# Kernel tuning notes

Measured on AMD Instinct MI355X. Metric: run time of the kernel, lower is better.

## Reference

```python
import jax, jax.numpy as jnp
import numpy as np

NUM_HEADS = 16
TEMPERATURE = 0.2


def setup_inputs() -> dict:
    key = jax.random.key(0)
    ks = jax.random.split(key, 6)
    B, TGT, SRC, D = 8, 256, 512, 1024
    seqs = jax.random.normal(ks[0], (B, TGT, D), jnp.float32)
    keys = jax.random.normal(ks[1], (B, SRC, D), jnp.float32)
    scale = 1.0 / np.sqrt(D).astype(np.float32)
    q_w = jax.random.normal(ks[2], (D, D), jnp.float32) * scale
    q_b = jax.random.normal(ks[3], (D,), jnp.float32) * 0.01
    k_w = jax.random.normal(ks[4], (D, D), jnp.float32) * scale
    k_b = jax.random.normal(ks[5], (D,), jnp.float32) * 0.01
    energy_bias = jnp.full((1,), -0.5, jnp.float32)
    return {"seqs": seqs, "keys": keys, "q_w": q_w, "q_b": q_b,
            "k_w": k_w, "k_b": k_b, "energy_bias": energy_bias}


def _monotonic_alignment(p):
    # p: (BH, tgt, src). Faithful to torch: T_i = triu(cumprod(1 - triu(roll(p_i),1)))
    # but T is built per target step inside a scan instead of materializing
    # the full (BH, tgt, src, src) tensor.
    BH, T, S = p.shape
    idx = jnp.arange(S)
    mask_strict = idx[None, :] > idx[:, None]   # triu(1)
    mask_ge = idx[None, :] >= idx[:, None]      # triu(0)
    p_roll = jnp.roll(p, 1, axis=-1)

    def step_T(pr_i):  # pr_i: (BH, S) -> (BH, S, S)
        pe = jnp.where(mask_strict, pr_i[:, None, :], 0.0)
        return jnp.where(mask_ge, jnp.cumprod(1.0 - pe, axis=-1), 0.0)

    T0 = step_T(p_roll[:, 0])
    alpha0 = p[:, 0] * T0[:, 0, :]              # (BH, S)

    def scan_fn(alpha, xs):
        p_i, pr_i = xs
        Ti = step_T(pr_i)                        # (BH, S, S)
        alpha_new = p_i * jnp.einsum('bm,bmn->bn', alpha, Ti)
        return alpha_new, alpha_new

    _, alphas = jax.lax.scan(
        scan_fn, alpha0,
        (jnp.swapaxes(p[:, 1:], 0, 1), jnp.swapaxes(p_roll[:, 1:], 0, 1)))
    return jnp.concatenate([alpha0[:, None], jnp.swapaxes(alphas, 0, 1)], axis=1)


def reference(seqs, keys, q_w, q_b, k_w, k_b, energy_bias):
    B, TGT, D = seqs.shape
    SRC = keys.shape[1]
    H = NUM_HEADS
    dh = D // H
    # EnergyProjection with num_layers=1: Linear + ReLU
    q = jax.nn.relu(seqs @ q_w.T + q_b)
    k = jax.nn.relu(keys @ k_w.T + k_b)
    q = q.reshape(B, TGT, H, dh).transpose(0, 2, 1, 3)   # (B,H,tgt,dh)
    k = k.reshape(B, SRC, H, dh).transpose(0, 2, 1, 3)   # (B,H,src,dh)
    energy = jnp.einsum('bhtd,bhsd->bhts', q, k) * (dh ** -0.5) + energy_bias[0]
    p_choose = jax.nn.sigmoid(energy / TEMPERATURE)       # (B,H,tgt,src)
    alpha = _monotonic_alignment(p_choose.reshape(B * H, TGT, SRC))
    alpha = alpha.reshape(B, H, TGT, SRC)
    return p_choose, alpha
```

## Files before the change

kernel.cpp:

```cpp
#include <hip/hip_runtime.h>

#define B_   8
#define TGT_ 256
#define SRC_ 512
#define D_   1024
#define H_   16
#define DH_  64

typedef _Float16 half4 __attribute__((ext_vector_type(4)));
typedef _Float16 half8 __attribute__((ext_vector_type(8)));
typedef float    floatx4 __attribute__((ext_vector_type(4)));

template <int CTRL>
__device__ __forceinline__ float dppf(float x) {
    return __int_as_float(__builtin_amdgcn_update_dpp(
        0, __float_as_int(x), CTRL, 0xF, 0xF, true));
}
__device__ __forceinline__ float rdlane(float x, int lane) {
    return __int_as_float(__builtin_amdgcn_readlane(__float_as_int(x), lane));
}

__global__ __launch_bounds__(256) void proj_fused_kernel(
    const float* __restrict__ seqs, const float* __restrict__ keys,
    const float* __restrict__ q_w,  const float* __restrict__ k_w,
    const float* __restrict__ q_b,  const float* __restrict__ k_b,
    _Float16* __restrict__ Qh, _Float16* __restrict__ Kh)
{
    __shared__ _Float16 As[128 * 32];
    __shared__ _Float16 Ws[64 * 32];

    const int tid = threadIdx.x;
    const int bx  = blockIdx.x;
    const int K   = D_;
    const int N   = D_;

    const float* A; const float* W; const float* bias; _Float16* C;
    int bm0;
    if (bx < 16) { A = seqs; W = q_w; bias = q_b; C = Qh; bm0 = bx * 128; }
    else         { A = keys; W = k_w; bias = k_b; C = Kh; bm0 = (bx - 16) * 128; }
    const int bn0 = blockIdx.y * 64;

    const int lrow = tid >> 3;
    const int lkc  = (tid & 7) * 4;
    const float* aG = A + (size_t)(bm0 + lrow) * K + lkc;
    const float* wG = W + (size_t)(bn0 + lrow) * K + lkc;
    _Float16* aL = As + tid * 4;
    _Float16* wL = Ws + tid * 4;

    float4 ra[4], rw[2];
#define PROJ_LOAD(k0)                                                       \
    {                                                                       \
        ra[0] = *(const float4*)(aG + (k0));                                \
        ra[1] = *(const float4*)(aG + (size_t)32 * K + (k0));               \
        ra[2] = *(const float4*)(aG + (size_t)64 * K + (k0));               \
        ra[3] = *(const float4*)(aG + (size_t)96 * K + (k0));               \
        rw[0] = *(const float4*)(wG + (k0));                                \
        rw[1] = *(const float4*)(wG + (size_t)32 * K + (k0));               \
    }

    floatx4 acc[4][2];
#pragma unroll
    for (int i = 0; i < 4; ++i)
#pragma unroll
        for (int j = 0; j < 2; ++j) acc[i][j] = (floatx4){0.f, 0.f, 0.f, 0.f};

    const int lane = tid & 63;
    const int wid  = tid >> 6;
    const int wm   = (wid >> 1) * 64;
    const int wn   = (wid & 1) * 32;
    const int fm   = lane & 15;
    const int fk   = (lane >> 4) * 8;
    const _Float16* aF = As + (wm + fm) * 32 + fk;
    const _Float16* bF = Ws + (wn + fm) * 32 + fk;

    PROJ_LOAD(0);

    for (int k0 = 0; k0 < K; k0 += 32) {
        __syncthreads();
#pragma unroll
        for (int i = 0; i < 4; ++i) {
            half4 h = { (_Float16)ra[i].x, (_Float16)ra[i].y,
                        (_Float16)ra[i].z, (_Float16)ra[i].w };
            *(half4*)(aL + i * 1024) = h;
        }
#pragma unroll
        for (int i = 0; i < 2; ++i) {
            half4 h = { (_Float16)rw[i].x, (_Float16)rw[i].y,
                        (_Float16)rw[i].z, (_Float16)rw[i].w };
            *(half4*)(wL + i * 1024) = h;
        }
        if (k0 + 32 < K) PROJ_LOAD(k0 + 32);
        __syncthreads();

        half8 a0 = *(const half8*)(aF);
        half8 a1 = *(const half8*)(aF + 16 * 32);
        half8 a2 = *(const half8*)(aF + 32 * 32);
        half8 a3 = *(const half8*)(aF + 48 * 32);
        half8 b0 = *(const half8*)(bF);
        half8 b1 = *(const half8*)(bF + 16 * 32);

        acc[0][0] = __builtin_amdgcn_mfma_f32_16x16x32_f16(a0, b0, acc[0][0], 0, 0, 0);
        acc[1][0] = __builtin_amdgcn_mfma_f32_16x16x32_f16(a1, b0, acc[1][0], 0, 0, 0);
        acc[2][0] = __builtin_amdgcn_mfma_f32_16x16x32_f16(a2, b0, acc[2][0], 0, 0, 0);
        acc[3][0] = __builtin_amdgcn_mfma_f32_16x16x32_f16(a3, b0, acc[3][0], 0, 0, 0);
        acc[0][1] = __builtin_amdgcn_mfma_f32_16x16x32_f16(a0, b1, acc[0][1], 0, 0, 0);
        acc[1][1] = __builtin_amdgcn_mfma_f32_16x16x32_f16(a1, b1, acc[1][1], 0, 0, 0);
        acc[2][1] = __builtin_amdgcn_mfma_f32_16x16x32_f16(a2, b1, acc[2][1], 0, 0, 0);
        acc[3][1] = __builtin_amdgcn_mfma_f32_16x16x32_f16(a3, b1, acc[3][1], 0, 0, 0);
    }

    const int er = (lane >> 4) * 4;
#pragma unroll
    for (int nt = 0; nt < 2; ++nt) {
        const int col = bn0 + wn + nt * 16 + fm;
        const float bv = bias[col];
#pragma unroll
        for (int mt = 0; mt < 4; ++mt) {
            const int row0 = bm0 + wm + mt * 16 + er;
#pragma unroll
            for (int r = 0; r < 4; ++r) {
                float v = acc[mt][nt][r] + bv;
                v = fmaxf(v, 0.0f);
                C[(size_t)(row0 + r) * N + col] = (_Float16)v;
            }
        }
    }
#undef PROJ_LOAD
}

__global__ __launch_bounds__(256) void energy_mfma_kernel(
    const _Float16* __restrict__ Q, const _Float16* __restrict__ K,
    const float* __restrict__ eb_ptr, float* __restrict__ P)
{
    __shared__ __align__(16) _Float16 Qt[2 * 64 * 32];
    __shared__ __align__(16) _Float16 Kt[2 * 128 * 32];

    const int tid = threadIdx.x;
    const int bh  = blockIdx.x;
    const int b   = bh >> 4;
    const int h   = bh & 15;
    const int t0  = blockIdx.y << 6;
    const int s0  = blockIdx.z << 7;

#pragma unroll
    for (int u = 0; u < 2; ++u) {
        const int unit = tid + u * 256;
        const int row = unit >> 3, hc = unit & 7;
        half8 v = *(const half8*)(Q + ((size_t)(b * TGT_ + t0 + row)) * D_ + h * DH_ + hc * 8);
        *(half8*)(Qt + (hc >> 2) * (64 * 32) + row * 32 + (hc & 3) * 8) = v;
    }
#pragma unroll
    for (int u = 0; u < 4; ++u) {
        const int unit = tid + u * 256;
        const int row = unit >> 3, hc = unit & 7;
        half8 v = *(const half8*)(K + ((size_t)(b * SRC_ + s0 + row)) * D_ + h * DH_ + hc * 8);
        *(half8*)(Kt + (hc >> 2) * (128 * 32) + row * 32 + (hc & 3) * 8) = v;
    }
    __syncthreads();

    const int lane = tid & 63;
    const int wid  = tid >> 6;
    const int wm   = (wid >> 1) * 32;
    const int wn   = (wid & 1) * 64;
    const int fm   = lane & 15;
    const int fk   = (lane >> 4) * 8;

    floatx4 acc[2][4];
#pragma unroll
    for (int i = 0; i < 2; ++i)
#pragma unroll
        for (int j = 0; j < 4; ++j) acc[i][j] = (floatx4){0.f, 0.f, 0.f, 0.f};

#pragma unroll
    for (int ks = 0; ks < 2; ++ks) {
        const _Float16* aB = Qt + ks * (64 * 32) + (wm + fm) * 32 + fk;
        const _Float16* bB = Kt + ks * (128 * 32) + (wn + fm) * 32 + fk;
        half8 a0 = *(const half8*)(aB);
        half8 a1 = *(const half8*)(aB + 16 * 32);
        half8 b0 = *(const half8*)(bB);
        half8 b1 = *(const half8*)(bB + 16 * 32);
        half8 b2 = *(const half8*)(bB + 32 * 32);
        half8 b3 = *(const half8*)(bB + 48 * 32);
        acc[0][0] = __builtin_amdgcn_mfma_f32_16x16x32_f16(a0, b0, acc[0][0], 0, 0, 0);
        acc[0][1] = __builtin_amdgcn_mfma_f32_16x16x32_f16(a0, b1, acc[0][1], 0, 0, 0);
        acc[0][2] = __builtin_amdgcn_mfma_f32_16x16x32_f16(a0, b2, acc[0][2], 0, 0, 0);
        acc[0][3] = __builtin_amdgcn_mfma_f32_16x16x32_f16(a0, b3, acc[0][3], 0, 0, 0);
        acc[1][0] = __builtin_amdgcn_mfma_f32_16x16x32_f16(a1, b0, acc[1][0], 0, 0, 0);
        acc[1][1] = __builtin_amdgcn_mfma_f32_16x16x32_f16(a1, b1, acc[1][1], 0, 0, 0);
        acc[1][2] = __builtin_amdgcn_mfma_f32_16x16x32_f16(a1, b2, acc[1][2], 0, 0, 0);
        acc[1][3] = __builtin_amdgcn_mfma_f32_16x16x32_f16(a1, b3, acc[1][3], 0, 0, 0);
    }

    const float eb = eb_ptr[0];
    const int er = (lane >> 4) * 4;
#pragma unroll
    for (int mt = 0; mt < 2; ++mt) {
#pragma unroll
        for (int nt = 0; nt < 4; ++nt) {
            const int s = s0 + wn + nt * 16 + fm;
#pragma unroll
            for (int r = 0; r < 4; ++r) {
                const int t = t0 + wm + mt * 16 + er + r;
                float x = (acc[mt][nt][r] * 0.125f + eb) * 5.0f;
                float p = 1.0f / (1.0f + __expf(-x));
                P[((size_t)bh * TGT_ + t) * SRC_ + s] = p;
            }
        }
    }
}

__global__ __launch_bounds__(64) void align_kernel(
    const float* __restrict__ P, float* __restrict__ Alpha)
{
    const int bh   = blockIdx.x;
    const int lane = threadIdx.x;
    const float* prow = P + (size_t)bh * TGT_ * SRC_;
    float* arow       = Alpha + (size_t)bh * TGT_ * SRC_;
    const int n0 = lane << 3;

    float bprev[8];
#pragma unroll
    for (int j = 0; j < 8; ++j) bprev[j] = 0.0f;
    if (lane == 0) bprev[0] = 1.0f;

    float4 bufA[8], bufB[8];
#pragma unroll
    for (int j = 0; j < 8; ++j) {
        const float* r = prow + (size_t)j * SRC_ + n0;
        bufA[j] = *(const float4*)r;
        bufB[j] = *(const float4*)(r + 4);
    }

    for (int g = 0; g < TGT_ / 8; ++g) {
#pragma unroll
        for (int jj = 0; jj < 8; ++jj) {
            const int i = g * 8 + jj;
            float4 ca = bufA[jj], cb = bufB[jj];
            if (g < TGT_ / 8 - 1) {
                const float* r = prow + (size_t)(i + 8) * SRC_ + n0;
                bufA[jj] = *(const float4*)r;
                bufB[jj] = *(const float4*)(r + 4);
            }
            float pl[8] = {ca.x, ca.y, ca.z, ca.w, cb.x, cb.y, cb.z, cb.w};

            float pm1 = dppf<0x111>(pl[7]);
            {
                float r15 = rdlane(pl[7], 15);
                float r31 = rdlane(pl[7], 31);
                float r47 = rdlane(pl[7], 47);
                pm1 = (lane == 16) ? r15 : pm1;
                pm1 = (lane == 32) ? r31 : pm1;
                pm1 = (lane == 48) ? r47 : pm1;
            }
            float a[8];
            a[0] = (lane == 0) ? 0.0f : (1.0f - pm1);
#pragma unroll
            for (int j = 1; j < 8; ++j) a[j] = 1.0f - pl[j - 1];

            float Aj[8], Bj[8];
            float A = a[0], Bv = bprev[0];
            Aj[0] = A; Bj[0] = Bv;
#pragma unroll
            for (int j = 1; j < 8; ++j) {
                Bv = fmaf(a[j], Bv, bprev[j]);
                A  = a[j] * A;
                Aj[j] = A; Bj[j] = Bv;
            }

            float As_ = A, Bs = Bv;
            {
                float Ash, Bsh;
                Ash = dppf<0x111>(As_); Bsh = dppf<0x111>(Bs);
                Ash = ((lane & 15) >= 1) ? Ash : 1.0f;
                Bs  = fmaf(As_, Bsh, Bs); As_ = As_ * Ash;
                Ash = dppf<0x112>(As_); Bsh = dppf<0x112>(Bs);
                Ash = ((lane & 15) >= 2) ? Ash : 1.0f;
                Bs  = fmaf(As_, Bsh, Bs); As_ = As_ * Ash;
                Ash = dppf<0x114>(As_); Bsh = dppf<0x114>(Bs);
                Ash = ((lane & 15) >= 4) ? Ash : 1.0f;
                Bs  = fmaf(As_, Bsh, Bs); As_ = As_ * Ash;
                Ash = dppf<0x118>(As_); Bsh = dppf<0x118>(Bs);
                Ash = ((lane & 15) >= 8) ? Ash : 1.0f;
                Bs  = fmaf(As_, Bsh, Bs); As_ = As_ * Ash;
            }

            float PB;
            {
                float B15 = rdlane(Bs, 15);
                float A31 = rdlane(As_, 31), B31 = rdlane(Bs, 31);
                float B47 = rdlane(Bs, 47);
                float PB1 = B15;
                float PB2 = fmaf(A31, PB1, B31);
                float PB3 = fmaf(rdlane(As_, 47), PB2, B47);
                const int seg = lane >> 4;
                PB = (seg == 0) ? 0.0f : ((seg == 1) ? PB1 : ((seg == 2) ? PB2 : PB3));
            }

            float EA = dppf<0x111>(As_);
            float EB = dppf<0x111>(Bs);
            EA = (lane & 15) ? EA : 1.0f;
            float cin = fmaf(EA, PB, EB);

            float an[8];
#pragma unroll
            for (int j = 0; j < 8; ++j) {
                float c = fmaf(Aj[j], cin, Bj[j]);
                an[j] = pl[j] * c;
                bprev[j] = an[j];
            }
            float4 o0 = {an[0], an[1], an[2], an[3]};
            float4 o1 = {an[4], an[5], an[6], an[7]};
            float* dst = arow + (size_t)i * SRC_ + n0;
            *(float4*)dst       = o0;
            *(float4*)(dst + 4) = o1;
        }
    }
}

extern "C" void kernel_launch(void* const* d_in, const int* in_sizes, int n_in,
                              void* d_out, int out_size, void* d_ws, size_t ws_size,
                              hipStream_t stream) {
    const float* seqs = (const float*)d_in[0];
    const float* keys = (const float*)d_in[1];
    const float* q_w  = (const float*)d_in[2];
    const float* q_b  = (const float*)d_in[3];
    const float* k_w  = (const float*)d_in[4];
    const float* k_b  = (const float*)d_in[5];
    const float* eb   = (const float*)d_in[6];

    float* out   = (float*)d_out;
    float* P     = out;
    float* Alpha = out + (size_t)B_ * H_ * TGT_ * SRC_;

    _Float16* Qh = (_Float16*)d_ws;
    _Float16* Kh = Qh + (size_t)B_ * TGT_ * D_;

    {
        dim3 grid(48, D_ / 64);
        proj_fused_kernel<<<grid, 256, 0, stream>>>(seqs, keys, q_w, k_w,
                                                    q_b, k_b, Qh, Kh);
    }
    {
        dim3 grid(B_ * H_, TGT_ / 64, SRC_ / 128);
        energy_mfma_kernel<<<grid, 256, 0, stream>>>(Qh, Kh, eb, P);
    }
    align_kernel<<<dim3(B_ * H_), 64, 0, stream>>>(P, Alpha);
}
```

Baseline: 234.4 us.

## Pre-convert inputs to fp16, use async LDS loads, stage energy stores through LDS

A separate conversion kernel turns the inputs and weights into fp16. The projection GEMM then loads fp16 tiles straight into LDS with global_load_lds and uses a larger 128x128 tile with 4x4 MFMA accumulators per wave. The energy kernel now writes sigmoid outputs through an LDS transpose buffer so the global stores become coalesced float4 rows. These changes add an extra kernel launch and an extra round trip through memory for the converted inputs, and the projection loop no longer has register prefetch overlap.

Result: no change. 233.3 us (-0.5%).

```diff
diff --git a/kernel.cpp b/kernel.cpp
--- a/kernel.cpp
+++ b/kernel.cpp
@@ -11,6 +11,12 @@
 typedef _Float16 half8 __attribute__((ext_vector_type(8)));
 typedef float    floatx4 __attribute__((ext_vector_type(4)));
 
+__device__ __forceinline__ void async_ld16(const void* g, void* l) {
+    __builtin_amdgcn_global_load_lds(
+        (const __attribute__((address_space(1))) void*)g,
+        (__attribute__((address_space(3))) void*)l, 16, 0, 0);
+}
+
 template <int CTRL>
 __device__ __forceinline__ float dppf(float x) {
     return __int_as_float(__builtin_amdgcn_update_dpp(
@@ -20,98 +26,93 @@
     return __int_as_float(__builtin_amdgcn_readlane(__float_as_int(x), lane));
 }
 
-__global__ __launch_bounds__(256) void proj_fused_kernel(
-    const float* __restrict__ seqs, const float* __restrict__ keys,
-    const float* __restrict__ q_w,  const float* __restrict__ k_w,
-    const float* __restrict__ q_b,  const float* __restrict__ k_b,
+__global__ __launch_bounds__(256) void cvt_kernel(
+    const float* __restrict__ s0, const float* __restrict__ s1,
+    const float* __restrict__ s2, const float* __restrict__ s3,
+    _Float16* __restrict__ d0, _Float16* __restrict__ d1,
+    _Float16* __restrict__ d2, _Float16* __restrict__ d3)
+{
+    const int bid = blockIdx.x;
+    const float* src; _Float16* dst; int base;
+    if      (bid < 2048) { src = s0; dst = d0; base = bid;        }
+    else if (bid < 6144) { src = s1; dst = d1; base = bid - 2048; }
+    else if (bid < 7168) { src = s2; dst = d2; base = bid - 6144; }
+    else                 { src = s3; dst = d3; base = bid - 7168; }
+    const int idx = (base * 256 + threadIdx.x) * 4;
+    float4 v = *(const float4*)(src + idx);
+    half4 o = { (_Float16)v.x, (_Float16)v.y, (_Float16)v.z, (_Float16)v.w };
+    *(half4*)(dst + idx) = o;
+}
+
+__global__ __launch_bounds__(256, 2) void proj_mfma_kernel(
+    const _Float16* __restrict__ seqs_h, const _Float16* __restrict__ keys_h,
+    const _Float16* __restrict__ qw_h,   const _Float16* __restrict__ kw_h,
+    const float* __restrict__ q_b,       const float* __restrict__ k_b,
     _Float16* __restrict__ Qh, _Float16* __restrict__ Kh)
 {
-    __shared__ _Float16 As[128 * 32];
-    __shared__ _Float16 Ws[64 * 32];
+    __shared__ __align__(16) _Float16 As[128 * 32];
+    __shared__ __align__(16) _Float16 Ws[128 * 32];
 
     const int tid = threadIdx.x;
     const int bx  = blockIdx.x;
-    const int K   = D_;
-    const int N   = D_;
-
-    const float* A; const float* W; const float* bias; _Float16* C;
+    const int K   = D_, N = D_;
+
+    const _Float16* A; const _Float16* W; const float* bias; _Float16* C;
     int bm0;
-    if (bx < 16) { A = seqs; W = q_w; bias = q_b; C = Qh; bm0 = bx * 128; }
-    else         { A = keys; W = k_w; bias = k_b; C = Kh; bm0 = (bx - 16) * 128; }
-    const int bn0 = blockIdx.y * 64;
-
-    const int lrow = tid >> 3;
-    const int lkc  = (tid & 7) * 4;
-    const float* aG = A + (size_t)(bm0 + lrow) * K + lkc;
-    const float* wG = W + (size_t)(bn0 + lrow) * K + lkc;
-    _Float16* aL = As + tid * 4;
-    _Float16* wL = Ws + tid * 4;
-
-    float4 ra[4], rw[2];
-#define PROJ_LOAD(k0)                                                       \
-    {                                                                       \
-        ra[0] = *(const float4*)(aG + (k0));                                \
-        ra[1] = *(const float4*)(aG + (size_t)32 * K + (k0));               \
-        ra[2] = *(const float4*)(aG + (size_t)64 * K + (k0));               \
-        ra[3] = *(const float4*)(aG + (size_t)96 * K + (k0));               \
-        rw[0] = *(const float4*)(wG + (k0));                                \
-        rw[1] = *(const float4*)(wG + (size_t)32 * K + (k0));               \
-    }
-
-    floatx4 acc[4][2];
+    if (bx < 16) { A = seqs_h; W = qw_h; bias = q_b; C = Qh; bm0 = bx * 128; }
+    else         { A = keys_h; W = kw_h; bias = k_b; C = Kh; bm0 = (bx - 16) * 128; }
+    const int bn0 = blockIdx.y * 128;
+
+    const int c0 = tid, c1 = tid + 256;
+    const _Float16* gA0 = A + (size_t)(bm0 + (c0 >> 2)) * K + (c0 & 3) * 8;
+    const _Float16* gA1 = A + (size_t)(bm0 + (c1 >> 2)) * K + (c1 & 3) * 8;
+    const _Float16* gW0 = W + (size_t)(bn0 + (c0 >> 2)) * K + (c0 & 3) * 8;
+    const _Float16* gW1 = W + (size_t)(bn0 + (c1 >> 2)) * K + (c1 & 3) * 8;
+    _Float16* lA0 = As + c0 * 8;
+    _Float16* lA1 = As + c1 * 8;
+    _Float16* lW0 = Ws + c0 * 8;
+    _Float16* lW1 = Ws + c1 * 8;
+
+    floatx4 acc[4][4];
 #pragma unroll
     for (int i = 0; i < 4; ++i)
 #pragma unroll
-        for (int j = 0; j < 2; ++j) acc[i][j] = (floatx4){0.f, 0.f, 0.f, 0.f};
+        for (int j = 0; j < 4; ++j) acc[i][j] = (floatx4){0.f, 0.f, 0.f, 0.f};
 
     const int lane = tid & 63;
     const int wid  = tid >> 6;
     const int wm   = (wid >> 1) * 64;
-    const int wn   = (wid & 1) * 32;
+    const int wn   = (wid & 1) * 64;
     const int fm   = lane & 15;
     const int fk   = (lane >> 4) * 8;
     const _Float16* aF = As + (wm + fm) * 32 + fk;
     const _Float16* bF = Ws + (wn + fm) * 32 + fk;
 
-    PROJ_LOAD(0);
-
     for (int k0 = 0; k0 < K; k0 += 32) {
         __syncthreads();
+        async_ld16(gA0 + k0, lA0);
+        async_ld16(gA1 + k0, lA1);
+        async_ld16(gW0 + k0, lW0);
+        async_ld16(gW1 + k0, lW1);
+        __syncthreads();
+
+        half8 a[4], b[4];
 #pragma unroll
         for (int i = 0; i < 4; ++i) {
-            half4 h = { (_Float16)ra[i].x, (_Float16)ra[i].y,
-                        (_Float16)ra[i].z, (_Float16)ra[i].w };
-            *(half4*)(aL + i * 1024) = h;
+            a[i] = *(const half8*)(aF + i * 16 * 32);
+            b[i] = *(const half8*)(bF + i * 16 * 32);
         }
 #pragma unroll
-        for (int i = 0; i < 2; ++i) {
-            half4 h = { (_Float16)rw[i].x, (_Float16)rw[i].y,
-                        (_Float16)rw[i].z, (_Float16)rw[i].w };
-            *(half4*)(wL + i * 1024) = h;
-        }
-        if (k0 + 32 < K) PROJ_LOAD(k0 + 32);
-        __syncthreads();
-
-        half8 a0 = *(const half8*)(aF);
-        half8 a1 = *(const half8*)(aF + 16 * 32);
-        half8 a2 = *(const half8*)(aF + 32 * 32);
-        half8 a3 = *(const half8*)(aF + 48 * 32);
-        half8 b0 = *(const half8*)(bF);
-        half8 b1 = *(const half8*)(bF + 16 * 32);
-
-        acc[0][0] = __builtin_amdgcn_mfma_f32_16x16x32_f16(a0, b0, acc[0][0], 0, 0, 0);
-        acc[1][0] = __builtin_amdgcn_mfma_f32_16x16x32_f16(a1, b0, acc[1][0], 0, 0, 0);
-        acc[2][0] = __builtin_amdgcn_mfma_f32_16x16x32_f16(a2, b0, acc[2][0], 0, 0, 0);
-        acc[3][0] = __builtin_amdgcn_mfma_f32_16x16x32_f16(a3, b0, acc[3][0], 0, 0, 0);
-        acc[0][1] = __builtin_amdgcn_mfma_f32_16x16x32_f16(a0, b1, acc[0][1], 0, 0, 0);
-        acc[1][1] = __builtin_amdgcn_mfma_f32_16x16x32_f16(a1, b1, acc[1][1], 0, 0, 0);
-        acc[2][1] = __builtin_amdgcn_mfma_f32_16x16x32_f16(a2, b1, acc[2][1], 0, 0, 0);
-        acc[3][1] = __builtin_amdgcn_mfma_f32_16x16x32_f16(a3, b1, acc[3][1], 0, 0, 0);
+        for (int mt = 0; mt < 4; ++mt)
+#pragma unroll
+            for (int nt = 0; nt < 4; ++nt)
+                acc[mt][nt] = __builtin_amdgcn_mfma_f32_16x16x32_f16(
+                    a[mt], b[nt], acc[mt][nt], 0, 0, 0);
     }
 
     const int er = (lane >> 4) * 4;
 #pragma unroll
-    for (int nt = 0; nt < 2; ++nt) {
+    for (int nt = 0; nt < 4; ++nt) {
         const int col = bn0 + wn + nt * 16 + fm;
         const float bv = bias[col];
 #pragma unroll
@@ -125,15 +126,16 @@
             }
         }
     }
-#undef PROJ_LOAD
-}
-
-__global__ __launch_bounds__(256) void energy_mfma_kernel(
+}
+
+__global__ __launch_bounds__(256, 4) void energy_mfma_kernel(
     const _Float16* __restrict__ Q, const _Float16* __restrict__ K,
     const float* __restrict__ eb_ptr, float* __restrict__ P)
 {
-    __shared__ __align__(16) _Float16 Qt[2 * 64 * 32];
-    __shared__ __align__(16) _Float16 Kt[2 * 128 * 32];
+    __shared__ __align__(16) unsigned char smem[64 * 132 * 4];
+    _Float16* Qt = (_Float16*)smem;
+    _Float16* Kt = Qt + 2 * 64 * 32;
+    float*    pT = (float*)smem;
 
     const int tid = threadIdx.x;
     const int bh  = blockIdx.x;
@@ -191,25 +193,36 @@
         acc[1][3] = __builtin_amdgcn_mfma_f32_16x16x32_f16(a1, b3, acc[1][3], 0, 0, 0);
     }
 
+    __syncthreads();
+
     const float eb = eb_ptr[0];
     const int er = (lane >> 4) * 4;
 #pragma unroll
     for (int mt = 0; mt < 2; ++mt) {
 #pragma unroll
         for (int nt = 0; nt < 4; ++nt) {
-            const int s = s0 + wn + nt * 16 + fm;
+            const int s_b = wn + nt * 16 + fm;
 #pragma unroll
             for (int r = 0; r < 4; ++r) {
-                const int t = t0 + wm + mt * 16 + er + r;
+                const int t_b = wm + mt * 16 + er + r;
                 float x = (acc[mt][nt][r] * 0.125f + eb) * 5.0f;
                 float p = 1.0f / (1.0f + __expf(-x));
-                P[((size_t)bh * TGT_ + t) * SRC_ + s] = p;
+                pT[t_b * 132 + s_b] = p;
             }
         }
     }
-}
-
-__global__ __launch_bounds__(64) void align_kernel(
+    __syncthreads();
+
+#pragma unroll
+    for (int u0 = 0; u0 < 8; ++u0) {
+        const int u = tid + u0 * 256;
+        const int row = u >> 5, c = u & 31;
+        float4 v = *(const float4*)&pT[row * 132 + c * 4];
+        *(float4*)&P[((size_t)bh * TGT_ + t0 + row) * SRC_ + s0 + c * 4] = v;
+    }
+}
+
+__global__ __launch_bounds__(64, 1) void align_kernel(
     const float* __restrict__ P, float* __restrict__ Alpha)
 {
     const int bh   = blockIdx.x;
@@ -236,7 +249,7 @@
         for (int jj = 0; jj < 8; ++jj) {
             const int i = g * 8 + jj;
             float4 ca = bufA[jj], cb = bufB[jj];
-            if (g < TGT_ / 8 - 1) {
+            if (i + 8 < TGT_) {
                 const float* r = prow + (size_t)(i + 8) * SRC_ + n0;
                 bufA[jj] = *(const float4*)r;
                 bufB[jj] = *(const float4*)(r + 4);
@@ -332,13 +345,19 @@
     float* P     = out;
     float* Alpha = out + (size_t)B_ * H_ * TGT_ * SRC_;
 
-    _Float16* Qh = (_Float16*)d_ws;
-    _Float16* Kh = Qh + (size_t)B_ * TGT_ * D_;
-
+    _Float16* Qh     = (_Float16*)d_ws;
+    _Float16* Kh     = Qh + (size_t)B_ * TGT_ * D_;
+    _Float16* seqs_h = Kh + (size_t)B_ * SRC_ * D_;
+    _Float16* keys_h = seqs_h + (size_t)B_ * TGT_ * D_;
+    _Float16* qw_h   = keys_h + (size_t)B_ * SRC_ * D_;
+    _Float16* kw_h   = qw_h + (size_t)D_ * D_;
+
+    cvt_kernel<<<dim3(8192), 256, 0, stream>>>(seqs, keys, q_w, k_w,
+                                               seqs_h, keys_h, qw_h, kw_h);
     {
-        dim3 grid(48, D_ / 64);
-        proj_fused_kernel<<<grid, 256, 0, stream>>>(seqs, keys, q_w, k_w,
-                                                    q_b, k_b, Qh, Kh);
+        dim3 grid(48, D_ / 128);
+        proj_mfma_kernel<<<grid, 256, 0, stream>>>(seqs_h, keys_h, qw_h, kw_h,
+                                                   q_b, k_b, Qh, Kh);
     }
     {
         dim3 grid(B_ * H_, TGT_ / 64, SRC_ / 128);
```
